# Kernel tuning notes

Measured on AMD Instinct MI355X. Metric: run time of the kernel, lower is better.

## Reference

```python
import jax, jax.numpy as jnp
import numpy as np

BATCH, TIME, IN, HID = 32, 512, 512, 1024
THRESHOLD = 1.0
BETA = 1.0 / 2.0  # 1/tau


def setup_inputs() -> dict:
    key = jax.random.key(0)
    kx, kw, kb = jax.random.split(key, 3)
    x = jax.random.normal(kx, (BATCH, TIME, IN), dtype=jnp.float32)
    bound = 1.0 / np.sqrt(IN)  # nn.Linear default init range
    W = jax.random.uniform(kw, (HID, IN), minval=-bound, maxval=bound, dtype=jnp.float32)
    b = jax.random.uniform(kb, (HID,), minval=-bound, maxval=bound, dtype=jnp.float32)
    return {"x": x, "W": W, "b": b}


def reference(x, W, b):
    # Precompute all per-step linear projections in one big GEMM: [B,T,H]
    hidden = jnp.einsum("bti,hi->bth", x, W) + b

    def step(mem, h_t):
        # h_t: [B,H]
        mem = BETA * mem + h_t
        spk = (mem > THRESHOLD).astype(h_t.dtype)
        mem = mem * (1.0 - spk)  # hard reset
        return mem, spk

    mem0 = jnp.zeros((x.shape[0], W.shape[0]), dtype=x.dtype)
    # scan over time: [T,B,H]
    _, spikes = jax.lax.scan(step, mem0, jnp.swapaxes(hidden, 0, 1))
    return jnp.swapaxes(spikes, 0, 1)  # [B,T,H]
```

## Files before the change

### kernel.cpp

```cpp
#include <hip/hip_runtime.h>

#define BATCH 32
#define TIME  512
#define INF   512
#define HIDF  1024

#define MBT  128
#define NBH  128
#define KCH  16
#define NCH  (INF / KCH)
#define TILEF (MBT * KCH)

#define GLD16(g, l) __builtin_amdgcn_global_load_lds(                      \
    (const __attribute__((address_space(1))) void*)(g),                    \
    (__attribute__((address_space(3))) void*)(l), 16, 0, 0)

__global__ __launch_bounds__(256, 3)
void snn_gemm_seqfma(const float* __restrict__ x, const float* __restrict__ W,
                     const float* __restrict__ bias, float* __restrict__ hidden) {
    __shared__ __align__(16) float xs[2 * TILEF];
    __shared__ __align__(16) float ws[2 * TILEF];

    const int tid = threadIdx.x;
    const int l   = tid & 63;
    const int wv  = __builtin_amdgcn_readfirstlane(tid >> 6);
    const int lx  = l & 7;
    const int ly  = (l >> 3) & 7;
    const int bt0 = blockIdx.y * MBT;
    const int h0  = blockIdx.x * NBH;
    const int wbt = 64 * (wv >> 1);
    const int wh  = 64 * (wv & 1);

    const int rl   = l >> 2;
    const int qs   = l & 3;
    const int rowA = 32 * wv + rl;
    const int rowB = rowA + 16;
    const int qA   = qs ^ ((rowA >> 3) & 3);
    const int qB   = qs ^ ((rowB >> 3) & 3);
    const float* xgA = x + (size_t)(bt0 + rowA) * INF + qA * 4;
    const float* xgB = x + (size_t)(bt0 + rowB) * INF + qB * 4;
    const float* wgA = W + (size_t)(h0 + rowA) * INF + qA * 4;
    const float* wgB = W + (size_t)(h0 + rowB) * INF + qB * 4;
    const int dOffA = (32 * wv) * KCH;
    const int dOffB = dOffA + 16 * KCH;

    GLD16(xgA, xs + dOffA);
    GLD16(xgB, xs + dOffB);
    GLD16(wgA, ws + dOffA);
    GLD16(wgB, ws + dOffB);

    float acc[8][8];
    #pragma unroll
    for (int r = 0; r < 8; ++r)
        #pragma unroll
        for (int c = 0; c < 8; ++c) acc[r][c] = 0.0f;

    __syncthreads();

    for (int kc = 0; kc < NCH; ++kc) {
        const int p  = kc & 1;
        const int np = p ^ 1;

        if (kc + 1 < NCH) {
            const int so = (kc + 1) * KCH;
            float* xd = xs + np * TILEF;
            float* wd = ws + np * TILEF;
            GLD16(xgA + so, xd + dOffA);
            GLD16(xgB + so, xd + dOffB);
            GLD16(wgA + so, wd + dOffA);
            GLD16(wgB + so, wd + dOffB);
        }

        const float* xb = xs + p * TILEF;
        const float* wb = ws + p * TILEF;
        #pragma unroll
        for (int g = 0; g < 4; ++g) {
            const int gx_ = (g ^ (ly & 3)) * 4;
            const int gw_ = (g ^ (lx & 3)) * 4;
            float4 xf[8], wf[8];
            #pragma unroll
            for (int r = 0; r < 8; ++r)
                xf[r] = *(const float4*)(xb + (wbt + ly * 8 + r) * KCH + gx_);
            #pragma unroll
            for (int c = 0; c < 8; ++c)
                wf[c] = *(const float4*)(wb + (wh + lx * 8 + c) * KCH + gw_);
            #pragma unroll
            for (int r = 0; r < 8; ++r)
                #pragma unroll
                for (int c = 0; c < 8; ++c)
                    acc[r][c] = __fmaf_rn(xf[r].x, wf[c].x, acc[r][c]);
            #pragma unroll
            for (int r = 0; r < 8; ++r)
                #pragma unroll
                for (int c = 0; c < 8; ++c)
                    acc[r][c] = __fmaf_rn(xf[r].y, wf[c].y, acc[r][c]);
            #pragma unroll
            for (int r = 0; r < 8; ++r)
                #pragma unroll
                for (int c = 0; c < 8; ++c)
                    acc[r][c] = __fmaf_rn(xf[r].z, wf[c].z, acc[r][c]);
            #pragma unroll
            for (int r = 0; r < 8; ++r)
                #pragma unroll
                for (int c = 0; c < 8; ++c)
                    acc[r][c] = __fmaf_rn(xf[r].w, wf[c].w, acc[r][c]);
        }
        __syncthreads();
    }

    float bv[8];
    #pragma unroll
    for (int c = 0; c < 8; ++c) bv[c] = bias[h0 + wh + lx * 8 + c];
    #pragma unroll
    for (int r = 0; r < 8; ++r) {
        float* orow = hidden + (size_t)(bt0 + wbt + ly * 8 + r) * HIDF
                             + h0 + wh + lx * 8;
        float4 o0, o1;
        o0.x = __fadd_rn(acc[r][0], bv[0]);
        o0.y = __fadd_rn(acc[r][1], bv[1]);
        o0.z = __fadd_rn(acc[r][2], bv[2]);
        o0.w = __fadd_rn(acc[r][3], bv[3]);
        o1.x = __fadd_rn(acc[r][4], bv[4]);
        o1.y = __fadd_rn(acc[r][5], bv[5]);
        o1.z = __fadd_rn(acc[r][6], bv[6]);
        o1.w = __fadd_rn(acc[r][7], bv[7]);
        ((float4*)orow)[0] = o0;
        ((float4*)orow)[1] = o1;
    }
}

__global__ __launch_bounds__(256)
void snn_scan_np(float* __restrict__ io) {
    const int n = blockIdx.x * 256 + threadIdx.x;
    const int b = n >> 10;
    const int h = n & 1023;
    float* p = io + (size_t)b * TIME * HIDF + h;

    float mem = 0.0f;
    for (int tb = 0; tb < TIME / 64; ++tb) {
        float hv[64];
        #pragma unroll
        for (int u = 0; u < 64; ++u) hv[u] = p[(size_t)(tb * 64 + u) * HIDF];
        float sp[64];
        #pragma unroll
        for (int u = 0; u < 64; ++u) {
            mem = __fadd_rn(__fmul_rn(0.5f, mem), hv[u]);
            bool s = mem > 1.0f;
            sp[u] = s ? 1.0f : 0.0f;
            if (s) mem = 0.0f;
        }
        #pragma unroll
        for (int u = 0; u < 64; ++u) p[(size_t)(tb * 64 + u) * HIDF] = sp[u];
    }
}

extern "C" void kernel_launch(void* const* d_in, const int* in_sizes, int n_in,
                              void* d_out, int out_size, void* d_ws, size_t ws_size,
                              hipStream_t stream) {
    const float* x    = (const float*)d_in[0];
    const float* W    = (const float*)d_in[1];
    const float* bias = (const float*)d_in[2];
    float* out = (float*)d_out;

    dim3 g1(HIDF / NBH, (BATCH * TIME) / MBT);
    snn_gemm_seqfma<<<g1, 256, 0, stream>>>(x, W, bias, out);

    snn_scan_np<<<(BATCH * HIDF) / 256, 256, 0, stream>>>(out);
}
```

Before: 330.1 us.

## Double-buffer LDS fragments in GEMM and software-pipeline scan loads

In the GEMM inner loop, LDS fragment loads for the next k-group are now issued before the FMAs of the current group, using two register buffers. This is meant to hide LDS latency, and launch bounds drop from 3 to 2 waves per EU to leave room for the extra registers. The scan kernel now uses 64-thread blocks, which spreads the 32768 threads over more CUs. It also double-buffers 32-step time segments so loads for the next segment overlap the recurrence, and spike stores are written directly instead of being staged. The risks are lower occupancy in the GEMM and register pressure from the doubled fragment buffers.

```diff
diff --git a/kernel.cpp b/kernel.cpp
--- a/kernel.cpp
+++ b/kernel.cpp
@@ -15,7 +15,48 @@
     (const __attribute__((address_space(1))) void*)(g),                    \
     (__attribute__((address_space(3))) void*)(l), 16, 0, 0)
 
-__global__ __launch_bounds__(256, 3)
+
+__device__ __forceinline__ void ldg_frag(const float* __restrict__ xb,
+                                         const float* __restrict__ wb,
+                                         int wbt, int wh, int lx, int ly, int g,
+                                         float4* __restrict__ xf,
+                                         float4* __restrict__ wf) {
+    const int gx_ = (g ^ (ly & 3)) * 4;
+    const int gw_ = (g ^ (lx & 3)) * 4;
+    #pragma unroll
+    for (int r = 0; r < 8; ++r)
+        xf[r] = *(const float4*)(xb + (wbt + ly * 8 + r) * KCH + gx_);
+    #pragma unroll
+    for (int c = 0; c < 8; ++c)
+        wf[c] = *(const float4*)(wb + (wh + lx * 8 + c) * KCH + gw_);
+}
+
+__device__ __forceinline__ void fma_frag(float acc[8][8],
+                                         const float4* __restrict__ xf,
+                                         const float4* __restrict__ wf) {
+    #pragma unroll
+    for (int r = 0; r < 8; ++r)
+        #pragma unroll
+        for (int c = 0; c < 8; ++c)
+            acc[r][c] = __fmaf_rn(xf[r].x, wf[c].x, acc[r][c]);
+    #pragma unroll
+    for (int r = 0; r < 8; ++r)
+        #pragma unroll
+        for (int c = 0; c < 8; ++c)
+            acc[r][c] = __fmaf_rn(xf[r].y, wf[c].y, acc[r][c]);
+    #pragma unroll
+    for (int r = 0; r < 8; ++r)
+        #pragma unroll
+        for (int c = 0; c < 8; ++c)
+            acc[r][c] = __fmaf_rn(xf[r].z, wf[c].z, acc[r][c]);
+    #pragma unroll
+    for (int r = 0; r < 8; ++r)
+        #pragma unroll
+        for (int c = 0; c < 8; ++c)
+            acc[r][c] = __fmaf_rn(xf[r].w, wf[c].w, acc[r][c]);
+}
+
+__global__ __launch_bounds__(256, 2)
 void snn_gemm_seqfma(const float* __restrict__ x, const float* __restrict__ W,
                      const float* __restrict__ bias, float* __restrict__ hidden) {
     __shared__ __align__(16) float xs[2 * TILEF];
@@ -73,38 +114,16 @@
 
         const float* xb = xs + p * TILEF;
         const float* wb = ws + p * TILEF;
-        #pragma unroll
-        for (int g = 0; g < 4; ++g) {
-            const int gx_ = (g ^ (ly & 3)) * 4;
-            const int gw_ = (g ^ (lx & 3)) * 4;
-            float4 xf[8], wf[8];
-            #pragma unroll
-            for (int r = 0; r < 8; ++r)
-                xf[r] = *(const float4*)(xb + (wbt + ly * 8 + r) * KCH + gx_);
-            #pragma unroll
-            for (int c = 0; c < 8; ++c)
-                wf[c] = *(const float4*)(wb + (wh + lx * 8 + c) * KCH + gw_);
-            #pragma unroll
-            for (int r = 0; r < 8; ++r)
-                #pragma unroll
-                for (int c = 0; c < 8; ++c)
-                    acc[r][c] = __fmaf_rn(xf[r].x, wf[c].x, acc[r][c]);
-            #pragma unroll
-            for (int r = 0; r < 8; ++r)
-                #pragma unroll
-                for (int c = 0; c < 8; ++c)
-                    acc[r][c] = __fmaf_rn(xf[r].y, wf[c].y, acc[r][c]);
-            #pragma unroll
-            for (int r = 0; r < 8; ++r)
-                #pragma unroll
-                for (int c = 0; c < 8; ++c)
-                    acc[r][c] = __fmaf_rn(xf[r].z, wf[c].z, acc[r][c]);
-            #pragma unroll
-            for (int r = 0; r < 8; ++r)
-                #pragma unroll
-                for (int c = 0; c < 8; ++c)
-                    acc[r][c] = __fmaf_rn(xf[r].w, wf[c].w, acc[r][c]);
-        }
+        float4 xa[8], wa[8], xc[8], wc[8];
+        ldg_frag(xb, wb, wbt, wh, lx, ly, 0, xa, wa);
+        ldg_frag(xb, wb, wbt, wh, lx, ly, 1, xc, wc);
+        fma_frag(acc, xa, wa);
+        ldg_frag(xb, wb, wbt, wh, lx, ly, 2, xa, wa);
+        fma_frag(acc, xc, wc);
+        ldg_frag(xb, wb, wbt, wh, lx, ly, 3, xc, wc);
+        fma_frag(acc, xa, wa);
+        fma_frag(acc, xc, wc);
+
         __syncthreads();
     }
 
@@ -129,28 +148,42 @@
     }
 }
 
-__global__ __launch_bounds__(256)
+#define SEG 32
+
+__global__ __launch_bounds__(64)
 void snn_scan_np(float* __restrict__ io) {
-    const int n = blockIdx.x * 256 + threadIdx.x;
+    const int n = blockIdx.x * 64 + threadIdx.x;
     const int b = n >> 10;
     const int h = n & 1023;
     float* p = io + (size_t)b * TIME * HIDF + h;
 
+    float A[SEG], B[SEG];
     float mem = 0.0f;
-    for (int tb = 0; tb < TIME / 64; ++tb) {
-        float hv[64];
-        #pragma unroll
-        for (int u = 0; u < 64; ++u) hv[u] = p[(size_t)(tb * 64 + u) * HIDF];
-        float sp[64];
-        #pragma unroll
-        for (int u = 0; u < 64; ++u) {
-            mem = __fadd_rn(__fmul_rn(0.5f, mem), hv[u]);
-            bool s = mem > 1.0f;
-            sp[u] = s ? 1.0f : 0.0f;
+
+    #pragma unroll
+    for (int u = 0; u < SEG; ++u) A[u] = p[u * HIDF];
+
+    for (int tb = 0; tb < TIME / SEG; tb += 2) {
+        #pragma unroll
+        for (int u = 0; u < SEG; ++u) B[u] = p[((tb + 1) * SEG + u) * HIDF];
+        #pragma unroll
+        for (int u = 0; u < SEG; ++u) {
+            mem = __fadd_rn(__fmul_rn(0.5f, mem), A[u]);
+            const bool s = mem > 1.0f;
+            p[(tb * SEG + u) * HIDF] = s ? 1.0f : 0.0f;
             if (s) mem = 0.0f;
         }
-        #pragma unroll
-        for (int u = 0; u < 64; ++u) p[(size_t)(tb * 64 + u) * HIDF] = sp[u];
+        if (tb + 2 < TIME / SEG) {
+            #pragma unroll
+            for (int u = 0; u < SEG; ++u) A[u] = p[((tb + 2) * SEG + u) * HIDF];
+        }
+        #pragma unroll
+        for (int u = 0; u < SEG; ++u) {
+            mem = __fadd_rn(__fmul_rn(0.5f, mem), B[u]);
+            const bool s = mem > 1.0f;
+            p[((tb + 1) * SEG + u) * HIDF] = s ? 1.0f : 0.0f;
+            if (s) mem = 0.0f;
+        }
     }
 }
 
@@ -165,5 +198,5 @@
     dim3 g1(HIDF / NBH, (BATCH * TIME) / MBT);
     snn_gemm_seqfma<<<g1, 256, 0, stream>>>(x, W, bias, out);
 
-    snn_scan_np<<<(BATCH * HIDF) / 256, 256, 0, stream>>>(out);
-}
+    snn_scan_np<<<(BATCH * HIDF) / 64, 64, 0, stream>>>(out);
+}
```

After: 324.6 us. About the same (-1.7%).
